# Optimization experiments

Hardware: AMD Instinct MI355X
Metric: run time of the kernel (lower is better)

Reference implementation:

```python
import jax, jax.numpy as jnp
import numpy as np

NEG = -9e15
SLOPE = 0.02

def setup_inputs() -> dict:
    key = jax.random.key(0)
    k1, k2, k3, k4 = jax.random.split(key, 4)
    N, IN, OUT = 16384, 128, 64
    x = jax.random.normal(k1, (N, IN), dtype=jnp.float32)
    adj = jax.random.randint(k2, (N, N), 0, 2, dtype=jnp.int32)
    weight = jax.random.normal(k3, (IN, OUT), dtype=jnp.float32) * (1.0 / np.sqrt(IN))
    att_weight = jax.random.normal(k4, (2 * OUT, 1), dtype=jnp.float32) * (1.0 / np.sqrt(2 * OUT))
    return {"x": x, "adj": adj, "weight": weight, "att_weight": att_weight}

def reference(x, adj, weight, att_weight):
    out_feature = weight.shape[1]
    Wh = x @ weight                                   # [N, out]
    f_i = Wh @ att_weight[:out_feature, :]            # [N, 1] source term
    f_j = Wh @ att_weight[out_feature:, :]            # [N, 1] dest term
    e = f_i + f_j.T                                   # [N, N] additive scores
    e = jax.nn.leaky_relu(e, negative_slope=SLOPE)
    att = jnp.where(adj > 0, e, NEG)
    att = jax.nn.softmax(att, axis=1)                 # masked row softmax
    h_prime = att @ Wh                                # [N, out]
    return jax.nn.elu(h_prime)                        # concat=True -> elu
```

## Files before the change

kernel.cpp:

```cpp
#include <hip/hip_runtime.h>
#include <cstdint>
#include <cstddef>

#define GN   16384
#define GIN  128
#define GOUT 64
#define LOG2E 1.44269504088896340736f

typedef __attribute__((ext_vector_type(8))) short short8;
typedef __attribute__((ext_vector_type(4))) float f32x4;
typedef __attribute__((ext_vector_type(4))) int   int4v;

__device__ __forceinline__ unsigned short f2bf(float f) {
  unsigned u = __float_as_uint(f);
  return (unsigned short)((u + 0x8000u) >> 16);
}

__device__ __forceinline__ unsigned short f2bf_rne(float f) {
  unsigned u = __float_as_uint(f);
  u += 0x7FFFu + ((u >> 16) & 1u);
  return (unsigned short)(u >> 16);
}

__global__ __launch_bounds__(256) void prep_kernel(
    const float* __restrict__ x, const float* __restrict__ w,
    const float* __restrict__ aw, unsigned short* __restrict__ wpk,
    float* __restrict__ fs2, float* __restrict__ fd2)
{
  __shared__ float ws[GIN * GOUT];
  __shared__ float red[2][64][4];

  const int t = threadIdx.x;
  const int rb = blockIdx.x * 64;

  for (int i = t; i < (GIN * GOUT) / 4; i += 256)
    ((float4*)ws)[i] = ((const float4*)w)[i];
  __syncthreads();

  const int r = t & 63, s = t >> 6;
  const int row = rb + r;
  const float* xr = x + (size_t)row * GIN;

  float acc[16];
#pragma unroll
  for (int d = 0; d < 16; ++d) acc[d] = 0.f;

  for (int kk = 0; kk < GIN; kk += 4) {
    float4 xv = *(const float4*)(xr + kk);
    float xa[4] = {xv.x, xv.y, xv.z, xv.w};
#pragma unroll
    for (int u = 0; u < 4; ++u) {
#pragma unroll
      for (int d = 0; d < 16; ++d)
        acc[d] += xa[u] * ws[(kk + u) * GOUT + s * 16 + d];
    }
  }

  const int jc = row >> 5;
  const int qq = (row & 31) >> 3;
  const int tt = row & 7;
  float psrc = 0.f, pdst = 0.f;
#pragma unroll
  for (int d = 0; d < 16; ++d) {
    const int dg = s * 16 + d;
    psrc += acc[d] * aw[dg];
    pdst += acc[d] * aw[GOUT + dg];
    const int f = dg >> 4, n = dg & 15;
    wpk[(size_t)jc * 4096 + f * 1024 + (qq * 16 + n) * 8 + tt] = f2bf_rne(acc[d]);
  }
  red[0][r][s] = psrc;
  red[1][r][s] = pdst;
  __syncthreads();
  if (s == 0) {
    float a_ = red[0][r][0] + red[0][r][1] + red[0][r][2] + red[0][r][3];
    float b_ = red[1][r][0] + red[1][r][1] + red[1][r][2] + red[1][r][3];
    fs2[row] = a_ * LOG2E;
    fd2[row] = b_ * LOG2E;
  }
}

__global__ __launch_bounds__(256) void gat_main(
    const int* __restrict__ adj, const unsigned short* __restrict__ wpk,
    const float* __restrict__ fs2, const float* __restrict__ fd2,
    float* __restrict__ num, float* __restrict__ den)
{
  const int wave  = blockIdx.x * 4 + (threadIdx.x >> 6);
  const int lane  = threadIdx.x & 63;
  const int strip = wave & 511;
  const int chunk = wave >> 9;
  const int m = lane & 15;
  const int q = lane >> 4;
  const int row0 = strip * 32 + m;
  const int row1 = row0 + 16;

  const float fs0 = fs2[row0];
  const float fs1 = fs2[row1];
  const int CW = GN / 8;
  const int j0 = chunk * CW;

  const int4v*  __restrict__ arow0 = (const int4v*)(adj + (size_t)row0 * GN);
  const int4v*  __restrict__ arow1 = (const int4v*)(adj + (size_t)row1 * GN);
  const float4* __restrict__ fdv   = (const float4*)fd2;
  const short8* __restrict__ wpk8  = (const short8*)wpk;

  f32x4 acc0a = {0,0,0,0}, acc1a = {0,0,0,0}, acc2a = {0,0,0,0}, acc3a = {0,0,0,0};
  f32x4 acc0b = {0,0,0,0}, acc1b = {0,0,0,0}, acc2b = {0,0,0,0}, acc3b = {0,0,0,0};
  f32x4 accda = {0,0,0,0}, accdb = {0,0,0,0};

  short8 b_ones;
#pragma unroll
  for (int i = 0; i < 8; ++i) b_ones[i] = (short)0x3F80;

  auto pcalc = [&](int a, float fd, float fs) -> unsigned short {
    float sv = fs + fd;
    float lv = fmaxf(sv, 0.02f * sv);
    float pe = __builtin_amdgcn_exp2f(lv);
    pe = (a != 0) ? pe : 0.f;
    return f2bf(pe);
  };

  auto mk_af = [&](int4v aA, int4v aB, float4 fA, float4 fB, float fs) -> short8 {
    short8 af;
    af[0] = (short)pcalc(aA.x, fA.x, fs);
    af[1] = (short)pcalc(aA.y, fA.y, fs);
    af[2] = (short)pcalc(aA.z, fA.z, fs);
    af[3] = (short)pcalc(aA.w, fA.w, fs);
    af[4] = (short)pcalc(aB.x, fB.x, fs);
    af[5] = (short)pcalc(aB.y, fB.y, fs);
    af[6] = (short)pcalc(aB.z, fB.z, fs);
    af[7] = (short)pcalc(aB.w, fB.w, fs);
    return af;
  };

#pragma unroll 2
  for (int j = j0; j < j0 + CW; j += 32) {
    const int i4 = (j >> 2) + (q << 1);
    int4v a00 = __builtin_nontemporal_load(arow0 + i4);
    int4v a01 = __builtin_nontemporal_load(arow0 + i4 + 1);
    int4v a10 = __builtin_nontemporal_load(arow1 + i4);
    int4v a11 = __builtin_nontemporal_load(arow1 + i4 + 1);
    float4 f0 = fdv[i4];
    float4 f1 = fdv[i4 + 1];

    const short8* wb = wpk8 + (size_t)(j >> 5) * 512 + lane;
    short8 b0 = wb[0];
    short8 b1 = wb[128];
    short8 b2 = wb[256];
    short8 b3 = wb[384];

    short8 af0 = mk_af(a00, a01, f0, f1, fs0);
    short8 af1 = mk_af(a10, a11, f0, f1, fs1);

    acc0a = __builtin_amdgcn_mfma_f32_16x16x32_bf16(af0, b0, acc0a, 0, 0, 0);
    acc1a = __builtin_amdgcn_mfma_f32_16x16x32_bf16(af0, b1, acc1a, 0, 0, 0);
    acc2a = __builtin_amdgcn_mfma_f32_16x16x32_bf16(af0, b2, acc2a, 0, 0, 0);
    acc3a = __builtin_amdgcn_mfma_f32_16x16x32_bf16(af0, b3, acc3a, 0, 0, 0);
    accda = __builtin_amdgcn_mfma_f32_16x16x32_bf16(af0, b_ones, accda, 0, 0, 0);
    acc0b = __builtin_amdgcn_mfma_f32_16x16x32_bf16(af1, b0, acc0b, 0, 0, 0);
    acc1b = __builtin_amdgcn_mfma_f32_16x16x32_bf16(af1, b1, acc1b, 0, 0, 0);
    acc2b = __builtin_amdgcn_mfma_f32_16x16x32_bf16(af1, b2, acc2b, 0, 0, 0);
    acc3b = __builtin_amdgcn_mfma_f32_16x16x32_bf16(af1, b3, acc3b, 0, 0, 0);
    accdb = __builtin_amdgcn_mfma_f32_16x16x32_bf16(af1, b_ones, accdb, 0, 0, 0);
  }

  if (m == 0) {
#pragma unroll
    for (int r = 0; r < 4; ++r) {
      unsafeAtomicAdd(&den[strip * 32 + q * 4 + r],      accda[r]);
      unsafeAtomicAdd(&den[strip * 32 + 16 + q * 4 + r], accdb[r]);
    }
  }

  const int orow0 = strip * 32 + q * 4;
#pragma unroll
  for (int r = 0; r < 4; ++r) {
    float* nra = num + (size_t)(orow0 + r) * GOUT + m;
    unsafeAtomicAdd(nra + 0,  acc0a[r]);
    unsafeAtomicAdd(nra + 16, acc1a[r]);
    unsafeAtomicAdd(nra + 32, acc2a[r]);
    unsafeAtomicAdd(nra + 48, acc3a[r]);
    float* nrb = num + (size_t)(orow0 + 16 + r) * GOUT + m;
    unsafeAtomicAdd(nrb + 0,  acc0b[r]);
    unsafeAtomicAdd(nrb + 16, acc1b[r]);
    unsafeAtomicAdd(nrb + 32, acc2b[r]);
    unsafeAtomicAdd(nrb + 48, acc3b[r]);
  }
}

__global__ __launch_bounds__(256) void fin_kernel(
    const float* __restrict__ num, const float* __restrict__ den,
    float* __restrict__ out)
{
  const int g = blockIdx.x * 256 + threadIdx.x;
  if (g < GN * GOUT) {
    float v = num[g] / den[g >> 6];
    out[g] = (v > 0.f) ? v : expm1f(v);
  }
}

extern "C" void kernel_launch(void* const* d_in, const int* in_sizes, int n_in,
                              void* d_out, int out_size, void* d_ws, size_t ws_size,
                              hipStream_t stream) {
  const float* x   = (const float*)d_in[0];
  const int*   adj = (const int*)d_in[1];
  const float* w   = (const float*)d_in[2];
  const float* aw  = (const float*)d_in[3];
  float* out = (float*)d_out;

  float* num = (float*)d_ws;
  float* den = num + (size_t)GN * GOUT;
  float* fs2 = den + GN;
  float* fd2 = fs2 + GN;
  unsigned short* wpk = (unsigned short*)(fd2 + GN);

  hipMemsetAsync(num, 0, ((size_t)GN * GOUT + GN) * sizeof(float), stream);
  prep_kernel<<<GN / 64, 256, 0, stream>>>(x, w, aw, wpk, fs2, fd2);
  gat_main<<<(GN / 32) * 8 / 4, 256, 0, stream>>>(adj, wpk, fs2, fd2, num, den);
  fin_kernel<<<(GN * GOUT) / 256, 256, 0, stream>>>(num, den, out);
}
```

Baseline: 1.452 ms.

## Process 64 rows per wave and replace atomics with per-chunk partial buffers

After: 1.385 ms. -4.6%, faster.

```diff
diff --git a/kernel.cpp b/kernel.cpp
--- a/kernel.cpp
+++ b/kernel.cpp
@@ -5,6 +5,7 @@
 #define GN   16384
 #define GIN  128
 #define GOUT 64
+#define NCH  8
 #define LOG2E 1.44269504088896340736f
 
 typedef __attribute__((ext_vector_type(8))) short short8;
@@ -82,63 +83,74 @@
 __global__ __launch_bounds__(256) void gat_main(
     const int* __restrict__ adj, const unsigned short* __restrict__ wpk,
     const float* __restrict__ fs2, const float* __restrict__ fd2,
-    float* __restrict__ num, float* __restrict__ den)
+    float* __restrict__ nump, float* __restrict__ denp)
 {
   const int wave  = blockIdx.x * 4 + (threadIdx.x >> 6);
   const int lane  = threadIdx.x & 63;
-  const int strip = wave & 511;
-  const int chunk = wave >> 9;
+  const int strip = wave & 255;
+  const int chunk = wave >> 8;
   const int m = lane & 15;
   const int q = lane >> 4;
-  const int row0 = strip * 32 + m;
-  const int row1 = row0 + 16;
-
-  const float fs0 = fs2[row0];
-  const float fs1 = fs2[row1];
-  const int CW = GN / 8;
+
+  int   row[4];
+  float fs[4];
+  const int4v* __restrict__ arow[4];
+#pragma unroll
+  for (int g = 0; g < 4; ++g) {
+    row[g] = strip * 64 + g * 16 + m;
+    fs[g] = fs2[row[g]];
+    arow[g] = (const int4v*)(adj + (size_t)row[g] * GN);
+  }
+
+  const int CW = GN / NCH;
   const int j0 = chunk * CW;
-
-  const int4v*  __restrict__ arow0 = (const int4v*)(adj + (size_t)row0 * GN);
-  const int4v*  __restrict__ arow1 = (const int4v*)(adj + (size_t)row1 * GN);
-  const float4* __restrict__ fdv   = (const float4*)fd2;
-  const short8* __restrict__ wpk8  = (const short8*)wpk;
-
-  f32x4 acc0a = {0,0,0,0}, acc1a = {0,0,0,0}, acc2a = {0,0,0,0}, acc3a = {0,0,0,0};
-  f32x4 acc0b = {0,0,0,0}, acc1b = {0,0,0,0}, acc2b = {0,0,0,0}, acc3b = {0,0,0,0};
-  f32x4 accda = {0,0,0,0}, accdb = {0,0,0,0};
+  const float4* __restrict__ fdv  = (const float4*)fd2;
+  const short8* __restrict__ wpk8 = (const short8*)wpk;
+
+  f32x4 acc[4][4];
+  f32x4 accd[4];
+#pragma unroll
+  for (int g = 0; g < 4; ++g) {
+    accd[g] = (f32x4){0.f, 0.f, 0.f, 0.f};
+#pragma unroll
+    for (int b = 0; b < 4; ++b) acc[g][b] = (f32x4){0.f, 0.f, 0.f, 0.f};
+  }
 
   short8 b_ones;
 #pragma unroll
   for (int i = 0; i < 8; ++i) b_ones[i] = (short)0x3F80;
 
-  auto pcalc = [&](int a, float fd, float fs) -> unsigned short {
-    float sv = fs + fd;
+  auto pcalc = [&](int a, float fd, float fsv) -> unsigned short {
+    float sv = fsv + fd;
     float lv = fmaxf(sv, 0.02f * sv);
     float pe = __builtin_amdgcn_exp2f(lv);
     pe = (a != 0) ? pe : 0.f;
     return f2bf(pe);
   };
 
-  auto mk_af = [&](int4v aA, int4v aB, float4 fA, float4 fB, float fs) -> short8 {
+  auto mk_af = [&](int4v aA, int4v aB, float4 fA, float4 fB, float fsv) -> short8 {
     short8 af;
-    af[0] = (short)pcalc(aA.x, fA.x, fs);
-    af[1] = (short)pcalc(aA.y, fA.y, fs);
-    af[2] = (short)pcalc(aA.z, fA.z, fs);
-    af[3] = (short)pcalc(aA.w, fA.w, fs);
-    af[4] = (short)pcalc(aB.x, fB.x, fs);
-    af[5] = (short)pcalc(aB.y, fB.y, fs);
-    af[6] = (short)pcalc(aB.z, fB.z, fs);
-    af[7] = (short)pcalc(aB.w, fB.w, fs);
+    af[0] = (short)pcalc(aA.x, fA.x, fsv);
+    af[1] = (short)pcalc(aA.y, fA.y, fsv);
+    af[2] = (short)pcalc(aA.z, fA.z, fsv);
+    af[3] = (short)pcalc(aA.w, fA.w, fsv);
+    af[4] = (short)pcalc(aB.x, fB.x, fsv);
+    af[5] = (short)pcalc(aB.y, fB.y, fsv);
+    af[6] = (short)pcalc(aB.z, fB.z, fsv);
+    af[7] = (short)pcalc(aB.w, fB.w, fsv);
     return af;
   };
 
-#pragma unroll 2
+#pragma unroll 1
   for (int j = j0; j < j0 + CW; j += 32) {
     const int i4 = (j >> 2) + (q << 1);
-    int4v a00 = __builtin_nontemporal_load(arow0 + i4);
-    int4v a01 = __builtin_nontemporal_load(arow0 + i4 + 1);
-    int4v a10 = __builtin_nontemporal_load(arow1 + i4);
-    int4v a11 = __builtin_nontemporal_load(arow1 + i4 + 1);
+
+    int4v a0[4], a1[4];
+#pragma unroll
+    for (int g = 0; g < 4; ++g) {
+      a0[g] = __builtin_nontemporal_load(arow[g] + i4);
+      a1[g] = __builtin_nontemporal_load(arow[g] + i4 + 1);
+    }
     float4 f0 = fdv[i4];
     float4 f1 = fdv[i4 + 1];
 
@@ -148,54 +160,49 @@
     short8 b2 = wb[256];
     short8 b3 = wb[384];
 
-    short8 af0 = mk_af(a00, a01, f0, f1, fs0);
-    short8 af1 = mk_af(a10, a11, f0, f1, fs1);
-
-    acc0a = __builtin_amdgcn_mfma_f32_16x16x32_bf16(af0, b0, acc0a, 0, 0, 0);
-    acc1a = __builtin_amdgcn_mfma_f32_16x16x32_bf16(af0, b1, acc1a, 0, 0, 0);
-    acc2a = __builtin_amdgcn_mfma_f32_16x16x32_bf16(af0, b2, acc2a, 0, 0, 0);
-    acc3a = __builtin_amdgcn_mfma_f32_16x16x32_bf16(af0, b3, acc3a, 0, 0, 0);
-    accda = __builtin_amdgcn_mfma_f32_16x16x32_bf16(af0, b_ones, accda, 0, 0, 0);
-    acc0b = __builtin_amdgcn_mfma_f32_16x16x32_bf16(af1, b0, acc0b, 0, 0, 0);
-    acc1b = __builtin_amdgcn_mfma_f32_16x16x32_bf16(af1, b1, acc1b, 0, 0, 0);
-    acc2b = __builtin_amdgcn_mfma_f32_16x16x32_bf16(af1, b2, acc2b, 0, 0, 0);
-    acc3b = __builtin_amdgcn_mfma_f32_16x16x32_bf16(af1, b3, acc3b, 0, 0, 0);
-    accdb = __builtin_amdgcn_mfma_f32_16x16x32_bf16(af1, b_ones, accdb, 0, 0, 0);
-  }
-
-  if (m == 0) {
+#pragma unroll
+    for (int g = 0; g < 4; ++g) {
+      short8 af = mk_af(a0[g], a1[g], f0, f1, fs[g]);
+      acc[g][0] = __builtin_amdgcn_mfma_f32_16x16x32_bf16(af, b0, acc[g][0], 0, 0, 0);
+      acc[g][1] = __builtin_amdgcn_mfma_f32_16x16x32_bf16(af, b1, acc[g][1], 0, 0, 0);
+      acc[g][2] = __builtin_amdgcn_mfma_f32_16x16x32_bf16(af, b2, acc[g][2], 0, 0, 0);
+      acc[g][3] = __builtin_amdgcn_mfma_f32_16x16x32_bf16(af, b3, acc[g][3], 0, 0, 0);
+      accd[g]   = __builtin_amdgcn_mfma_f32_16x16x32_bf16(af, b_ones, accd[g], 0, 0, 0);
+    }
+  }
+
+  float* np = nump + (size_t)chunk * GN * GOUT;
+  float* dp = denp + (size_t)chunk * GN;
+#pragma unroll
+  for (int g = 0; g < 4; ++g) {
+    const int orow0 = strip * 64 + g * 16 + q * 4;
 #pragma unroll
     for (int r = 0; r < 4; ++r) {
-      unsafeAtomicAdd(&den[strip * 32 + q * 4 + r],      accda[r]);
-      unsafeAtomicAdd(&den[strip * 32 + 16 + q * 4 + r], accdb[r]);
-    }
-  }
-
-  const int orow0 = strip * 32 + q * 4;
-#pragma unroll
-  for (int r = 0; r < 4; ++r) {
-    float* nra = num + (size_t)(orow0 + r) * GOUT + m;
-    unsafeAtomicAdd(nra + 0,  acc0a[r]);
-    unsafeAtomicAdd(nra + 16, acc1a[r]);
-    unsafeAtomicAdd(nra + 32, acc2a[r]);
-    unsafeAtomicAdd(nra + 48, acc3a[r]);
-    float* nrb = num + (size_t)(orow0 + 16 + r) * GOUT + m;
-    unsafeAtomicAdd(nrb + 0,  acc0b[r]);
-    unsafeAtomicAdd(nrb + 16, acc1b[r]);
-    unsafeAtomicAdd(nrb + 32, acc2b[r]);
-    unsafeAtomicAdd(nrb + 48, acc3b[r]);
+      float* nr = np + (size_t)(orow0 + r) * GOUT + m;
+      __builtin_nontemporal_store(acc[g][0][r], nr + 0);
+      __builtin_nontemporal_store(acc[g][1][r], nr + 16);
+      __builtin_nontemporal_store(acc[g][2][r], nr + 32);
+      __builtin_nontemporal_store(acc[g][3][r], nr + 48);
+      if (m == 0) dp[orow0 + r] = accd[g][r];
+    }
   }
 }
 
 __global__ __launch_bounds__(256) void fin_kernel(
-    const float* __restrict__ num, const float* __restrict__ den,
+    const float* __restrict__ nump, const float* __restrict__ denp,
     float* __restrict__ out)
 {
   const int g = blockIdx.x * 256 + threadIdx.x;
-  if (g < GN * GOUT) {
-    float v = num[g] / den[g >> 6];
-    out[g] = (v > 0.f) ? v : expm1f(v);
-  }
+  if (g >= GN * GOUT) return;
+  const int row = g >> 6;
+  float s = 0.f, d = 0.f;
+#pragma unroll
+  for (int c = 0; c < NCH; ++c) {
+    s += nump[(size_t)c * GN * GOUT + g];
+    d += denp[(size_t)c * GN + row];
+  }
+  float v = s / d;
+  out[g] = (v > 0.f) ? v : expm1f(v);
 }
 
 extern "C" void kernel_launch(void* const* d_in, const int* in_sizes, int n_in,
@@ -207,14 +214,13 @@
   const float* aw  = (const float*)d_in[3];
   float* out = (float*)d_out;
 
-  float* num = (float*)d_ws;
-  float* den = num + (size_t)GN * GOUT;
-  float* fs2 = den + GN;
-  float* fd2 = fs2 + GN;
+  float* nump = (float*)d_ws;
+  float* denp = nump + (size_t)NCH * GN * GOUT;
+  float* fs2  = denp + (size_t)NCH * GN;
+  float* fd2  = fs2 + GN;
   unsigned short* wpk = (unsigned short*)(fd2 + GN);
 
-  hipMemsetAsync(num, 0, ((size_t)GN * GOUT + GN) * sizeof(float), stream);
   prep_kernel<<<GN / 64, 256, 0, stream>>>(x, w, aw, wpk, fs2, fd2);
-  gat_main<<<(GN / 32) * 8 / 4, 256, 0, stream>>>(adj, wpk, fs2, fd2, num, den);
-  fin_kernel<<<(GN * GOUT) / 256, 256, 0, stream>>>(num, den, out);
-}
+  gat_main<<<(GN / 64) * NCH / 4, 256, 0, stream>>>(adj, wpk, fs2, fd2, nump, denp);
+  fin_kernel<<<(GN * GOUT) / 256, 256, 0, stream>>>(nump, denp, out);
+}
```

## Give each wave full rows and fuse normalization and ELU into main kernel

Applied to the files above, without the earlier changes.

Result: slower. 1.553 ms (+6.9%).

```diff
diff --git a/kernel.cpp b/kernel.cpp
--- a/kernel.cpp
+++ b/kernel.cpp
@@ -82,36 +82,28 @@
 __global__ __launch_bounds__(256) void gat_main(
     const int* __restrict__ adj, const unsigned short* __restrict__ wpk,
     const float* __restrict__ fs2, const float* __restrict__ fd2,
-    float* __restrict__ num, float* __restrict__ den)
+    float* __restrict__ out)
 {
   const int wave  = blockIdx.x * 4 + (threadIdx.x >> 6);
   const int lane  = threadIdx.x & 63;
-  const int strip = wave & 511;
-  const int chunk = wave >> 9;
   const int m = lane & 15;
   const int q = lane >> 4;
-  const int row0 = strip * 32 + m;
-  const int row1 = row0 + 16;
+  const int row = wave * 16 + m;
 
-  const float fs0 = fs2[row0];
-  const float fs1 = fs2[row1];
-  const int CW = GN / 8;
-  const int j0 = chunk * CW;
+  const float fs = fs2[row];
 
-  const int4v*  __restrict__ arow0 = (const int4v*)(adj + (size_t)row0 * GN);
-  const int4v*  __restrict__ arow1 = (const int4v*)(adj + (size_t)row1 * GN);
-  const float4* __restrict__ fdv   = (const float4*)fd2;
-  const short8* __restrict__ wpk8  = (const short8*)wpk;
+  const int4v*  __restrict__ arow = (const int4v*)(adj + (size_t)row * GN);
+  const float4* __restrict__ fdv  = (const float4*)fd2;
+  const short8* __restrict__ wpk8 = (const short8*)wpk;
 
-  f32x4 acc0a = {0,0,0,0}, acc1a = {0,0,0,0}, acc2a = {0,0,0,0}, acc3a = {0,0,0,0};
-  f32x4 acc0b = {0,0,0,0}, acc1b = {0,0,0,0}, acc2b = {0,0,0,0}, acc3b = {0,0,0,0};
-  f32x4 accda = {0,0,0,0}, accdb = {0,0,0,0};
+  f32x4 acc0 = {0,0,0,0}, acc1 = {0,0,0,0}, acc2 = {0,0,0,0}, acc3 = {0,0,0,0};
+  f32x4 accd = {0,0,0,0};
 
   short8 b_ones;
 #pragma unroll
   for (int i = 0; i < 8; ++i) b_ones[i] = (short)0x3F80;
 
-  auto pcalc = [&](int a, float fd, float fs) -> unsigned short {
+  auto pcalc = [&](int a, float fd) -> unsigned short {
     float sv = fs + fd;
     float lv = fmaxf(sv, 0.02f * sv);
     float pe = __builtin_amdgcn_exp2f(lv);
@@ -119,26 +111,11 @@
     return f2bf(pe);
   };
 
-  auto mk_af = [&](int4v aA, int4v aB, float4 fA, float4 fB, float fs) -> short8 {
-    short8 af;
-    af[0] = (short)pcalc(aA.x, fA.x, fs);
-    af[1] = (short)pcalc(aA.y, fA.y, fs);
-    af[2] = (short)pcalc(aA.z, fA.z, fs);
-    af[3] = (short)pcalc(aA.w, fA.w, fs);
-    af[4] = (short)pcalc(aB.x, fB.x, fs);
-    af[5] = (short)pcalc(aB.y, fB.y, fs);
-    af[6] = (short)pcalc(aB.z, fB.z, fs);
-    af[7] = (short)pcalc(aB.w, fB.w, fs);
-    return af;
-  };
-
 #pragma unroll 2
-  for (int j = j0; j < j0 + CW; j += 32) {
+  for (int j = 0; j < GN; j += 32) {
     const int i4 = (j >> 2) + (q << 1);
-    int4v a00 = __builtin_nontemporal_load(arow0 + i4);
-    int4v a01 = __builtin_nontemporal_load(arow0 + i4 + 1);
-    int4v a10 = __builtin_nontemporal_load(arow1 + i4);
-    int4v a11 = __builtin_nontemporal_load(arow1 + i4 + 1);
+    int4v a0 = __builtin_nontemporal_load(arow + i4);
+    int4v a1 = __builtin_nontemporal_load(arow + i4 + 1);
     float4 f0 = fdv[i4];
     float4 f1 = fdv[i4 + 1];
 
@@ -148,53 +125,36 @@
     short8 b2 = wb[256];
     short8 b3 = wb[384];
 
-    short8 af0 = mk_af(a00, a01, f0, f1, fs0);
-    short8 af1 = mk_af(a10, a11, f0, f1, fs1);
+    short8 af;
+    af[0] = (short)pcalc(a0.x, f0.x);
+    af[1] = (short)pcalc(a0.y, f0.y);
+    af[2] = (short)pcalc(a0.z, f0.z);
+    af[3] = (short)pcalc(a0.w, f0.w);
+    af[4] = (short)pcalc(a1.x, f1.x);
+    af[5] = (short)pcalc(a1.y, f1.y);
+    af[6] = (short)pcalc(a1.z, f1.z);
+    af[7] = (short)pcalc(a1.w, f1.w);
 
-    acc0a = __builtin_amdgcn_mfma_f32_16x16x32_bf16(af0, b0, acc0a, 0, 0, 0);
-    acc1a = __builtin_amdgcn_mfma_f32_16x16x32_bf16(af0, b1, acc1a, 0, 0, 0);
-    acc2a = __builtin_amdgcn_mfma_f32_16x16x32_bf16(af0, b2, acc2a, 0, 0, 0);
-    acc3a = __builtin_amdgcn_mfma_f32_16x16x32_bf16(af0, b3, acc3a, 0, 0, 0);
-    accda = __builtin_amdgcn_mfma_f32_16x16x32_bf16(af0, b_ones, accda, 0, 0, 0);
-    acc0b = __builtin_amdgcn_mfma_f32_16x16x32_bf16(af1, b0, acc0b, 0, 0, 0);
-    acc1b = __builtin_amdgcn_mfma_f32_16x16x32_bf16(af1, b1, acc1b, 0, 0, 0);
-    acc2b = __builtin_amdgcn_mfma_f32_16x16x32_bf16(af1, b2, acc2b, 0, 0, 0);
-    acc3b = __builtin_amdgcn_mfma_f32_16x16x32_bf16(af1, b3, acc3b, 0, 0, 0);
-    accdb = __builtin_amdgcn_mfma_f32_16x16x32_bf16(af1, b_ones, accdb, 0, 0, 0);
+    acc0 = __builtin_amdgcn_mfma_f32_16x16x32_bf16(af, b0, acc0, 0, 0, 0);
+    acc1 = __builtin_amdgcn_mfma_f32_16x16x32_bf16(af, b1, acc1, 0, 0, 0);
+    acc2 = __builtin_amdgcn_mfma_f32_16x16x32_bf16(af, b2, acc2, 0, 0, 0);
+    acc3 = __builtin_amdgcn_mfma_f32_16x16x32_bf16(af, b3, acc3, 0, 0, 0);
+    accd = __builtin_amdgcn_mfma_f32_16x16x32_bf16(af, b_ones, accd, 0, 0, 0);
   }
 
-  if (m == 0) {
-#pragma unroll
-    for (int r = 0; r < 4; ++r) {
-      unsafeAtomicAdd(&den[strip * 32 + q * 4 + r],      accda[r]);
-      unsafeAtomicAdd(&den[strip * 32 + 16 + q * 4 + r], accdb[r]);
-    }
-  }
-
-  const int orow0 = strip * 32 + q * 4;
+  const int orow0 = wave * 16 + q * 4;
 #pragma unroll
   for (int r = 0; r < 4; ++r) {
-    float* nra = num + (size_t)(orow0 + r) * GOUT + m;
-    unsafeAtomicAdd(nra + 0,  acc0a[r]);
-    unsafeAtomicAdd(nra + 16, acc1a[r]);
-    unsafeAtomicAdd(nra + 32, acc2a[r]);
-    unsafeAtomicAdd(nra + 48, acc3a[r]);
-    float* nrb = num + (size_t)(orow0 + 16 + r) * GOUT + m;
-    unsafeAtomicAdd(nrb + 0,  acc0b[r]);
-    unsafeAtomicAdd(nrb + 16, acc1b[r]);
-    unsafeAtomicAdd(nrb + 32, acc2b[r]);
-    unsafeAtomicAdd(nrb + 48, acc3b[r]);
-  }
-}
-
-__global__ __launch_bounds__(256) void fin_kernel(
-    const float* __restrict__ num, const float* __restrict__ den,
-    float* __restrict__ out)
-{
-  const int g = blockIdx.x * 256 + threadIdx.x;
-  if (g < GN * GOUT) {
-    float v = num[g] / den[g >> 6];
-    out[g] = (v > 0.f) ? v : expm1f(v);
+    const float dv = accd[r];
+    float* orow = out + (size_t)(orow0 + r) * GOUT + m;
+    float v0 = acc0[r] / dv;
+    float v1 = acc1[r] / dv;
+    float v2 = acc2[r] / dv;
+    float v3 = acc3[r] / dv;
+    orow[0]  = (v0 > 0.f) ? v0 : expm1f(v0);
+    orow[16] = (v1 > 0.f) ? v1 : expm1f(v1);
+    orow[32] = (v2 > 0.f) ? v2 : expm1f(v2);
+    orow[48] = (v3 > 0.f) ? v3 : expm1f(v3);
   }
 }
 
@@ -207,14 +167,10 @@
   const float* aw  = (const float*)d_in[3];
   float* out = (float*)d_out;
 
-  float* num = (float*)d_ws;
-  float* den = num + (size_t)GN * GOUT;
-  float* fs2 = den + GN;
+  float* fs2 = (float*)d_ws;
   float* fd2 = fs2 + GN;
   unsigned short* wpk = (unsigned short*)(fd2 + GN);
 
-  hipMemsetAsync(num, 0, ((size_t)GN * GOUT + GN) * sizeof(float), stream);
   prep_kernel<<<GN / 64, 256, 0, stream>>>(x, w, aw, wpk, fs2, fd2);
-  gat_main<<<(GN / 32) * 8 / 4, 256, 0, stream>>>(adj, wpk, fs2, fd2, num, den);
-  fin_kernel<<<(GN * GOUT) / 256, 256, 0, stream>>>(num, den, out);
+  gat_main<<<256, 256, 0, stream>>>(adj, wpk, fs2, fd2, out);
 }
```
